# Optimization experiments

Hardware: AMD Instinct MI355X
Metric: run time of the kernel (lower is better)

Reference implementation:

```python
import jax, jax.numpy as jnp
import numpy as np

HIDDEN, INPUT_DIM, OUTPUT_DIM, SEQ_LEN, BATCH = 1024, 1, 10, 784, 512


def make_discrete_hippo(N, L):
    # HiPPO-LegS matrix: A[n,k] = -sqrt(2n+1)sqrt(2k+1) for n>k, -(n+1) on diag; B[n]=sqrt(2n+1)
    q = np.arange(N, dtype=np.float64)
    P = np.sqrt(1.0 + 2.0 * q)
    A = -(np.tril(np.outer(P, P)) - np.diag(q))
    B = P[:, None]  # (N, 1)
    # bilinear (Tustin) discretization with step = 1/L
    step = 1.0 / L
    I = np.eye(N)
    M = np.linalg.inv(I - (step / 2.0) * A)
    Ad = M @ (I + (step / 2.0) * A)
    Bd = step * (M @ B)
    return jnp.asarray(Ad, jnp.float32), jnp.asarray(Bd, jnp.float32)


def setup_inputs() -> dict:
    key = jax.random.key(0)
    k1, k2, k3 = jax.random.split(key, 3)
    x = jax.random.normal(k1, (BATCH, SEQ_LEN, 1), jnp.float32)
    # C: xavier_uniform-like scale, shape (input_dim, hidden_dim)
    C = jax.random.normal(k2, (INPUT_DIM, HIDDEN), jnp.float32) / np.sqrt(HIDDEN).astype(np.float32)
    # final Dense(output_dim): kernel (input_dim, output_dim), bias (output_dim,)
    W = jax.random.normal(k3, (INPUT_DIM, OUTPUT_DIM), jnp.float32)
    b = jnp.zeros((OUTPUT_DIM,), jnp.float32)
    return {"x": x, "C": C, "W": W, "b": b}


def reference(x, C, W, b):
    Ad, Bd = make_discrete_hippo(HIDDEN, SEQ_LEN)  # constants (not learned)
    AdT = Ad.T                       # (N, N)
    Bvec = Bd[:, 0]                  # (N,)
    us = jnp.moveaxis(x[..., 0], 1, 0)  # (seq, batch) -- scan over time axis
    h0 = jnp.zeros((x.shape[0], HIDDEN), x.dtype)

    def step(h, u):
        # h_next = tanh(A h^T + B u)^T  ==  tanh(h @ A^T + u[:,None]*B)
        h_next = jnp.tanh(h @ AdT + u[:, None] * Bvec[None, :])  # (batch, N)
        y = h_next @ C.T                                         # (batch, input_dim)
        return h_next, y

    _, ys = jax.lax.scan(step, h0, us)  # ys: (seq, batch, input_dim)
    # Dense applied to all timesteps then [:, -1, :] == Dense on last timestep
    return ys[-1] @ W + b  # (batch, output_dim)
```

## Files before the change

kernel.cpp:

```cpp
#include <hip/hip_runtime.h>
#include <math.h>


#define SEQ     784
#define OUT_DIM 10
#define NW      4
#define CH      16
#define NCH     (SEQ/CH)
#define EPL     4
#define NG      (EPL/2)

typedef float v2f __attribute__((ext_vector_type(2)));

#if __has_builtin(__builtin_elementwise_fma)
__device__ __forceinline__ v2f fma2(v2f a, v2f b, v2f c) {
    return __builtin_elementwise_fma(a, b, c);
}
#else
__device__ __forceinline__ v2f fma2(v2f a, v2f b, v2f c) {
    v2f r; r.x = fmaf(a.x, b.x, c.x); r.y = fmaf(a.y, b.y, c.y); return r;
}
#endif

#if __has_builtin(__builtin_amdgcn_exp2f)
#define EXP2F(x) __builtin_amdgcn_exp2f(x)
#else
#define EXP2F(x) __expf(0.69314718055994531f * (x))
#endif

template<int CTRL, int ROW_MASK>
__device__ __forceinline__ float dpp_mov(float src, float old) {
    return __int_as_float(__builtin_amdgcn_update_dpp(
        __float_as_int(old), __float_as_int(src), CTRL, ROW_MASK, 0xf, false));
}

__global__ __launch_bounds__(256, 2)
void ssm_hippo_scan(const float* __restrict__ x,
                    const float* __restrict__ C,
                    const float* __restrict__ W,
                    const float* __restrict__ bvec,
                    float* __restrict__ out)
{
    const int b    = blockIdx.x;
    const int tid  = threadIdx.x;
    const int wv   = tid >> 6;
    const int lane = tid & 63;

    __shared__ __align__(16) float u_s[SEQ];
    __shared__ __align__(16) float totB_s[NW-1][SEQ];
    __shared__ double part_s[NW];

    for (int t = tid; t < SEQ; t += 256) u_s[t] = x[b * SEQ + t];

    const double hdt  = 0.5 / (double)SEQ;
    const double L2E2 = 2.0 * 1.4426950408889634;

    v2f upc2[NG], nhdtP2[NG], pdin2[NG], invd2v[NG], aprod2[NG];
    v2f aprel2;
    float alphas[EPL], apH;
    float Alev0, Alev1, Alev2, Alev3, Alev4, Alev5, Aexcl;
    {
        double apd = 1.0;
#pragma unroll
        for (int i = 0; i < EPL; ++i) {
            const int    n = wv * 256 + lane * EPL + i;
            const double p = sqrt(1.0 + 2.0 * (double)n);
            const double d = 1.0 + hdt * (double)(n + 1);
            const double a = 1.0 - hdt * p * p / d;
            upc2[i>>1][i&1]   = (float)(L2E2 * hdt * p);
            nhdtP2[i>>1][i&1] = (float)(-hdt * p);
            pdin2[i>>1][i&1]  = (float)(p / d);
            invd2v[i>>1][i&1] = (float)(2.0 / d);
            alphas[i]         = (float)a;
            aprod2[i>>1][i&1] = (float)apd;
            apd *= a;
        }
        aprel2 = (v2f){1.0f, alphas[2]};
        apH    = alphas[2] * alphas[3];
        float A = (float)apd;
        Alev0 = A; A *= dpp_mov<0x111, 0xf>(A, 1.0f);
        Alev1 = A; A *= dpp_mov<0x112, 0xf>(A, 1.0f);
        Alev2 = A; A *= dpp_mov<0x114, 0xf>(A, 1.0f);
        Alev3 = A; A *= dpp_mov<0x118, 0xf>(A, 1.0f);
        Alev4 = A; A *= dpp_mov<0x142, 0xa>(A, 1.0f);
        Alev5 = A; A *= dpp_mov<0x143, 0xc>(A, 1.0f);
        Aexcl = dpp_mov<0x138, 0xf>(A, 1.0f);
    }

    float cF1 = 0.0f, cF2 = 0.0f, cF12 = 0.0f;
    {
        double n1 = 1.0, d1 = 1.0, n2 = 1.0, d2 = 1.0;
        for (int n = 256; n < 512; ++n) {
            n1 *= 1.0 - hdt * (double)n; d1 *= 1.0 + hdt * (double)(n + 1);
        }
        for (int n = 512; n < 768; ++n) {
            n2 *= 1.0 - hdt * (double)n; d2 *= 1.0 + hdt * (double)(n + 1);
        }
        const double Phi1 = n1 / d1, Phi2 = n2 / d2;
        cF1 = (float)Phi1; cF2 = (float)Phi2; cF12 = (float)(Phi1 * Phi2);
    }

    const float c2  = (float)L2E2;
    const float nc4 = (float)(-2.0 * L2E2);
    const float p4  = (float)(2.0 * L2E2);
    const v2f  c2v  = (v2f){c2, c2},  nc2v = (v2f){-c2, -c2};
    const v2f  nc4v = (v2f){nc4, nc4}, p4v = (v2f){p4, p4};

    __syncthreads();

    v2f r2[NG];
#pragma unroll
    for (int j = 0; j < NG; ++j) r2[j] = (v2f){0.5f, 0.5f};

#pragma unroll 1
    for (int tick = 0; tick < NCH + NW - 1; ++tick) {
        const int ch = tick - wv;
        if (0 <= ch && ch < NCH) {
            float4 u4[CH/4];
            float  Tin[CH];
            {
                const float4* up = (const float4*)&u_s[ch * CH];
#pragma unroll
                for (int q = 0; q < CH/4; ++q) u4[q] = up[q];
            }
            if (wv == 0) {
#pragma unroll
                for (int k = 0; k < CH; ++k) Tin[k] = 0.0f;
            } else if (wv == 1) {
                const float4* b0 = (const float4*)&totB_s[0][ch * CH];
#pragma unroll
                for (int q = 0; q < CH/4; ++q) {
                    const float4 v0 = b0[q];
                    Tin[4*q+0] = v0.x; Tin[4*q+1] = v0.y;
                    Tin[4*q+2] = v0.z; Tin[4*q+3] = v0.w;
                }
            } else if (wv == 2) {
                const float4* b0 = (const float4*)&totB_s[0][ch * CH];
                const float4* b1 = (const float4*)&totB_s[1][ch * CH];
#pragma unroll
                for (int q = 0; q < CH/4; ++q) {
                    const float4 v0 = b0[q], v1 = b1[q];
                    Tin[4*q+0] = fmaf(cF1, v0.x, v1.x);
                    Tin[4*q+1] = fmaf(cF1, v0.y, v1.y);
                    Tin[4*q+2] = fmaf(cF1, v0.z, v1.z);
                    Tin[4*q+3] = fmaf(cF1, v0.w, v1.w);
                }
            } else {
                const float4* b0 = (const float4*)&totB_s[0][ch * CH];
                const float4* b1 = (const float4*)&totB_s[1][ch * CH];
                const float4* b2 = (const float4*)&totB_s[2][ch * CH];
#pragma unroll
                for (int q = 0; q < CH/4; ++q) {
                    const float4 v0 = b0[q], v1 = b1[q], v2 = b2[q];
                    Tin[4*q+0] = fmaf(cF12, v0.x, fmaf(cF2, v1.x, v2.x));
                    Tin[4*q+1] = fmaf(cF12, v0.y, fmaf(cF2, v1.y, v2.y));
                    Tin[4*q+2] = fmaf(cF12, v0.z, fmaf(cF2, v1.z, v2.z));
                    Tin[4*q+3] = fmaf(cF12, v0.w, fmaf(cF2, v1.w, v2.w));
                }
            }
            float Bacc[CH];

#pragma unroll
            for (int k = 0; k < CH; ++k) {
                const float u  = ((const float*)&u4[k>>2])[k&3];
                const v2f  uu  = (v2f){u, u};

                v2f w2[NG], gam2[NG], negh[NG];
#pragma unroll
                for (int j = 0; j < NG; ++j) {
                    const v2f au = fma2(upc2[j], uu, c2v);
                    w2[j]   = fma2(nc4v, r2[j], au);
                    gam2[j] = pdin2[j] * w2[j];
                    negh[j] = fma2(p4v, r2[j], nc2v);
                }

                v2f Tb2[NG];
                Tb2[0] = (v2f){0.0f, gam2[0].x};
                const float Tl0 = fmaf(alphas[1], gam2[0].x, gam2[0].y);
                Tb2[1] = (v2f){0.0f, gam2[1].x};
                const float Tl1 = fmaf(alphas[3], gam2[1].x, gam2[1].y);
                Tb2[1] = fma2(aprel2, (v2f){Tl0, Tl0}, Tb2[1]);
                float B = fmaf(apH, Tl0, Tl1);

                float Bin;
                Bin = dpp_mov<0x111, 0xf>(B, 0.0f); B = fmaf(Alev0, Bin, B);
                Bin = dpp_mov<0x112, 0xf>(B, 0.0f); B = fmaf(Alev1, Bin, B);
                Bin = dpp_mov<0x114, 0xf>(B, 0.0f); B = fmaf(Alev2, Bin, B);
                Bin = dpp_mov<0x118, 0xf>(B, 0.0f); B = fmaf(Alev3, Bin, B);
                Bin = dpp_mov<0x142, 0xa>(B, 0.0f); B = fmaf(Alev4, Bin, B);
                Bin = dpp_mov<0x143, 0xc>(B, 0.0f); B = fmaf(Alev5, Bin, B);
                Bacc[k] = B;

                const float Tst  = dpp_mov<0x138, 0xf>(B, 0.0f);
                const float Tent = fmaf(Aexcl, Tin[k], Tst);
                const v2f  Tev   = (v2f){Tent, Tent};

                v2f Tn[NG], tmp[NG], g2l[NG], e[NG];
#pragma unroll
                for (int j = 0; j < NG; ++j) Tn[j]  = fma2(aprod2[j], Tev, Tb2[j]);
#pragma unroll
                for (int j = 0; j < NG; ++j) tmp[j] = fma2(nhdtP2[j], Tn[j], w2[j]);
#pragma unroll
                for (int j = 0; j < NG; ++j) g2l[j] = fma2(tmp[j], invd2v[j], negh[j]);
#pragma unroll
                for (int j = 0; j < NG; ++j) { e[j].x = EXP2F(g2l[j].x);
                                               e[j].y = EXP2F(g2l[j].y); }
#pragma unroll
                for (int j = 0; j < NG; ++j) e[j] = e[j] + (v2f){1.0f, 1.0f};
#pragma unroll
                for (int j = 0; j < NG; ++j) { r2[j].x = __builtin_amdgcn_rcpf(e[j].x);
                                               r2[j].y = __builtin_amdgcn_rcpf(e[j].y); }
            }

            if (wv < NW - 1 && lane == 63) {
                float4* tp = (float4*)&totB_s[wv][ch * CH];
#pragma unroll
                for (int q = 0; q < CH/4; ++q)
                    tp[q] = make_float4(Bacc[4*q], Bacc[4*q+1],
                                        Bacc[4*q+2], Bacc[4*q+3]);
            }
        }
        __syncthreads();
    }

    double acc = 0.0;
#pragma unroll
    for (int i = 0; i < EPL; ++i) {
        const float hi = fmaf(-2.0f, r2[i>>1][i&1], 1.0f);
        acc = fma((double)C[wv * 256 + lane * EPL + i], (double)hi, acc);
    }
#pragma unroll
    for (int off = 32; off > 0; off >>= 1)
        acc += __shfl_down(acc, off, 64);
    if (lane == 0) part_s[wv] = acc;
    __syncthreads();
    if (tid < OUT_DIM) {
        const double tot = part_s[0] + part_s[1] + part_s[2] + part_s[3];
        out[b * OUT_DIM + tid] =
            (float)fma(tot, (double)W[tid], (double)bvec[tid]);
    }
}

extern "C" void kernel_launch(void* const* d_in, const int* in_sizes, int n_in,
                              void* d_out, int out_size, void* d_ws, size_t ws_size,
                              hipStream_t stream) {
    const float* x  = (const float*)d_in[0];
    const float* C  = (const float*)d_in[1];
    const float* W  = (const float*)d_in[2];
    const float* bv = (const float*)d_in[3];
    float* out      = (float*)d_out;
    hipLaunchKernelGGL(ssm_hippo_scan, dim3(512), dim3(256), 0, stream,
                       x, C, W, bv, out);
}
```

Before: 265.8 us.

## Reformulate per-step recurrence with scaled state and shared reciprocal across four elements

Replaces the packed-float2 recurrence with a scalar reformulation: the state is kept as a scaled tanh value, and the intra-thread lower-triangular coupling is folded into precomputed coefficients. One reciprocal now serves four sigmoid denominators through product tricks, and most DPP moves switch to bound_ctrl broadcast. The aim is to cut transcendental and dependent-op count on the serial per-timestep critical path. In exchange it adds an fminf clamp before exp2 and gives up packed FMA. Combining four denominators into one product can also lose precision or overflow, which the clamp partly guards against.

```diff
diff --git a/kernel.cpp b/kernel.cpp
--- a/kernel.cpp
+++ b/kernel.cpp
@@ -8,19 +8,6 @@
 #define CH      16
 #define NCH     (SEQ/CH)
 #define EPL     4
-#define NG      (EPL/2)
-
-typedef float v2f __attribute__((ext_vector_type(2)));
-
-#if __has_builtin(__builtin_elementwise_fma)
-__device__ __forceinline__ v2f fma2(v2f a, v2f b, v2f c) {
-    return __builtin_elementwise_fma(a, b, c);
-}
-#else
-__device__ __forceinline__ v2f fma2(v2f a, v2f b, v2f c) {
-    v2f r; r.x = fmaf(a.x, b.x, c.x); r.y = fmaf(a.y, b.y, c.y); return r;
-}
-#endif
 
 #if __has_builtin(__builtin_amdgcn_exp2f)
 #define EXP2F(x) __builtin_amdgcn_exp2f(x)
@@ -32,6 +19,11 @@
 __device__ __forceinline__ float dpp_mov(float src, float old) {
     return __int_as_float(__builtin_amdgcn_update_dpp(
         __float_as_int(old), __float_as_int(src), CTRL, ROW_MASK, 0xf, false));
+}
+template<int CTRL>
+__device__ __forceinline__ float dpp_bc0(float src) {
+    return __int_as_float(__builtin_amdgcn_update_dpp(
+        0, __float_as_int(src), CTRL, 0xf, 0xf, true));
 }
 
 __global__ __launch_bounds__(256, 2)
@@ -55,29 +47,40 @@
     const double hdt  = 0.5 / (double)SEQ;
     const double L2E2 = 2.0 * 1.4426950408889634;
 
-    v2f upc2[NG], nhdtP2[NG], pdin2[NG], invd2v[NG], aprod2[NG];
-    v2f aprel2;
-    float alphas[EPL], apH;
+    float upc[EPL], ivd[EPL], ka[EPL], cB[EPL];
+    float t10, t20, t21, t30, t31, t32;
     float Alev0, Alev1, Alev2, Alev3, Alev4, Alev5, Aexcl;
+    float c2, n2c2;
     {
-        double apd = 1.0;
+        double p[EPL], d[EPL], a[EPL], pdin[EPL], hp[EPL];
 #pragma unroll
         for (int i = 0; i < EPL; ++i) {
-            const int    n = wv * 256 + lane * EPL + i;
-            const double p = sqrt(1.0 + 2.0 * (double)n);
-            const double d = 1.0 + hdt * (double)(n + 1);
-            const double a = 1.0 - hdt * p * p / d;
-            upc2[i>>1][i&1]   = (float)(L2E2 * hdt * p);
-            nhdtP2[i>>1][i&1] = (float)(-hdt * p);
-            pdin2[i>>1][i&1]  = (float)(p / d);
-            invd2v[i>>1][i&1] = (float)(2.0 / d);
-            alphas[i]         = (float)a;
-            aprod2[i>>1][i&1] = (float)apd;
-            apd *= a;
-        }
-        aprel2 = (v2f){1.0f, alphas[2]};
-        apH    = alphas[2] * alphas[3];
-        float A = (float)apd;
+            const int n = wv * 256 + lane * EPL + i;
+            p[i]    = sqrt(1.0 + 2.0 * (double)n);
+            d[i]    = 1.0 + hdt * (double)(n + 1);
+            a[i]    = 1.0 - hdt * p[i] * p[i] / d[i];
+            pdin[i] = p[i] / d[i];
+            hp[i]   = 2.0 * hdt * p[i] / d[i];
+            upc[i]  = (float)(L2E2 * hdt * p[i]);
+            ivd[i]  = (float)(2.0 / d[i]);
+        }
+        const double ap0 = 1.0, ap1 = a[0], ap2 = a[0]*a[1], ap3 = a[0]*a[1]*a[2];
+        ka[0] = (float)(-hp[0] * ap0);
+        ka[1] = (float)(-hp[1] * ap1);
+        ka[2] = (float)(-hp[2] * ap2);
+        ka[3] = (float)(-hp[3] * ap3);
+        cB[0] = (float)(a[1]*a[2]*a[3] * pdin[0]);
+        cB[1] = (float)(a[2]*a[3] * pdin[1]);
+        cB[2] = (float)(a[3] * pdin[2]);
+        cB[3] = (float)(pdin[3]);
+        t10 = (float)(-hp[1] * pdin[0]);
+        t20 = (float)(-hp[2] * a[1] * pdin[0]);
+        t21 = (float)(-hp[2] * pdin[1]);
+        t30 = (float)(-hp[3] * a[2] * a[1] * pdin[0]);
+        t31 = (float)(-hp[3] * a[2] * pdin[1]);
+        t32 = (float)(-hp[3] * pdin[2]);
+
+        float A = (float)(a[0]*a[1]*a[2]*a[3]);
         Alev0 = A; A *= dpp_mov<0x111, 0xf>(A, 1.0f);
         Alev1 = A; A *= dpp_mov<0x112, 0xf>(A, 1.0f);
         Alev2 = A; A *= dpp_mov<0x114, 0xf>(A, 1.0f);
@@ -85,6 +88,9 @@
         Alev4 = A; A *= dpp_mov<0x142, 0xa>(A, 1.0f);
         Alev5 = A; A *= dpp_mov<0x143, 0xc>(A, 1.0f);
         Aexcl = dpp_mov<0x138, 0xf>(A, 1.0f);
+
+        c2   = (float)L2E2;
+        n2c2 = (float)(-2.0 * L2E2);
     }
 
     float cF1 = 0.0f, cF2 = 0.0f, cF12 = 0.0f;
@@ -100,17 +106,9 @@
         cF1 = (float)Phi1; cF2 = (float)Phi2; cF12 = (float)(Phi1 * Phi2);
     }
 
-    const float c2  = (float)L2E2;
-    const float nc4 = (float)(-2.0 * L2E2);
-    const float p4  = (float)(2.0 * L2E2);
-    const v2f  c2v  = (v2f){c2, c2},  nc2v = (v2f){-c2, -c2};
-    const v2f  nc4v = (v2f){nc4, nc4}, p4v = (v2f){p4, p4};
-
     __syncthreads();
 
-    v2f r2[NG];
-#pragma unroll
-    for (int j = 0; j < NG; ++j) r2[j] = (v2f){0.5f, 0.5f};
+    float m0 = 0.0f, m1 = 0.0f, m2 = 0.0f, m3 = 0.0f;
 
 #pragma unroll 1
     for (int tick = 0; tick < NCH + NW - 1; ++tick) {
@@ -162,54 +160,55 @@
 
 #pragma unroll
             for (int k = 0; k < CH; ++k) {
-                const float u  = ((const float*)&u4[k>>2])[k&3];
-                const v2f  uu  = (v2f){u, u};
-
-                v2f w2[NG], gam2[NG], negh[NG];
-#pragma unroll
-                for (int j = 0; j < NG; ++j) {
-                    const v2f au = fma2(upc2[j], uu, c2v);
-                    w2[j]   = fma2(nc4v, r2[j], au);
-                    gam2[j] = pdin2[j] * w2[j];
-                    negh[j] = fma2(p4v, r2[j], nc2v);
-                }
-
-                v2f Tb2[NG];
-                Tb2[0] = (v2f){0.0f, gam2[0].x};
-                const float Tl0 = fmaf(alphas[1], gam2[0].x, gam2[0].y);
-                Tb2[1] = (v2f){0.0f, gam2[1].x};
-                const float Tl1 = fmaf(alphas[3], gam2[1].x, gam2[1].y);
-                Tb2[1] = fma2(aprel2, (v2f){Tl0, Tl0}, Tb2[1]);
-                float B = fmaf(apH, Tl0, Tl1);
+                const float u = ((const float*)&u4[k>>2])[k&3];
+
+                const float w0 = fmaf(upc[0], u, m0);
+                const float w1 = fmaf(upc[1], u, m1);
+                const float w2 = fmaf(upc[2], u, m2);
+                const float w3 = fmaf(upc[3], u, m3);
+
+                float B = fmaf(cB[0], w0,
+                          fmaf(cB[1], w1,
+                          fmaf(cB[2], w2, cB[3] * w3)));
 
                 float Bin;
-                Bin = dpp_mov<0x111, 0xf>(B, 0.0f); B = fmaf(Alev0, Bin, B);
-                Bin = dpp_mov<0x112, 0xf>(B, 0.0f); B = fmaf(Alev1, Bin, B);
-                Bin = dpp_mov<0x114, 0xf>(B, 0.0f); B = fmaf(Alev2, Bin, B);
-                Bin = dpp_mov<0x118, 0xf>(B, 0.0f); B = fmaf(Alev3, Bin, B);
+                Bin = dpp_bc0<0x111>(B);            B = fmaf(Alev0, Bin, B);
+                Bin = dpp_bc0<0x112>(B);            B = fmaf(Alev1, Bin, B);
+                Bin = dpp_bc0<0x114>(B);            B = fmaf(Alev2, Bin, B);
+                Bin = dpp_bc0<0x118>(B);            B = fmaf(Alev3, Bin, B);
                 Bin = dpp_mov<0x142, 0xa>(B, 0.0f); B = fmaf(Alev4, Bin, B);
                 Bin = dpp_mov<0x143, 0xc>(B, 0.0f); B = fmaf(Alev5, Bin, B);
                 Bacc[k] = B;
 
-                const float Tst  = dpp_mov<0x138, 0xf>(B, 0.0f);
+                const float Tst  = dpp_bc0<0x138>(B);
                 const float Tent = fmaf(Aexcl, Tin[k], Tst);
-                const v2f  Tev   = (v2f){Tent, Tent};
-
-                v2f Tn[NG], tmp[NG], g2l[NG], e[NG];
-#pragma unroll
-                for (int j = 0; j < NG; ++j) Tn[j]  = fma2(aprod2[j], Tev, Tb2[j]);
-#pragma unroll
-                for (int j = 0; j < NG; ++j) tmp[j] = fma2(nhdtP2[j], Tn[j], w2[j]);
-#pragma unroll
-                for (int j = 0; j < NG; ++j) g2l[j] = fma2(tmp[j], invd2v[j], negh[j]);
-#pragma unroll
-                for (int j = 0; j < NG; ++j) { e[j].x = EXP2F(g2l[j].x);
-                                               e[j].y = EXP2F(g2l[j].y); }
-#pragma unroll
-                for (int j = 0; j < NG; ++j) e[j] = e[j] + (v2f){1.0f, 1.0f};
-#pragma unroll
-                for (int j = 0; j < NG; ++j) { r2[j].x = __builtin_amdgcn_rcpf(e[j].x);
-                                               r2[j].y = __builtin_amdgcn_rcpf(e[j].y); }
+
+                const float b0g = fmaf(ivd[0], w0, -m0);
+                const float b1g = fmaf(ivd[1], w1, -m1);
+                const float b2g = fmaf(ivd[2], w2, -m2);
+                const float b3g = fmaf(ivd[3], w3, -m3);
+                const float g0 = fmaf(ka[0], Tent, b0g);
+                const float g1 = fmaf(ka[1], Tent, fmaf(t10, w0, b1g));
+                const float g2 = fmaf(ka[2], Tent,
+                                 fmaf(t20, w0, fmaf(t21, w1, b2g)));
+                const float g3 = fmaf(ka[3], Tent,
+                                 fmaf(t30, w0,
+                                 fmaf(t31, w1, fmaf(t32, w2, b3g))));
+
+                const float e0 = EXP2F(fminf(g0, 30.0f));
+                const float e1 = EXP2F(fminf(g1, 30.0f));
+                const float e2 = EXP2F(fminf(g2, 30.0f));
+                const float e3 = EXP2F(fminf(g3, 30.0f));
+                const float q0 = e0 + 1.0f, q1 = e1 + 1.0f;
+                const float q2 = e2 + 1.0f, q3 = e3 + 1.0f;
+                const float p01 = q0 * q1, p23 = q2 * q3;
+                const float ip  = __builtin_amdgcn_rcpf(p01 * p23);
+                const float i01 = p23 * ip;
+                const float i23 = p01 * ip;
+                m0 = fmaf(n2c2, q1 * i01, c2);
+                m1 = fmaf(n2c2, q0 * i01, c2);
+                m2 = fmaf(n2c2, q3 * i23, c2);
+                m3 = fmaf(n2c2, q2 * i23, c2);
             }
 
             if (wv < NW - 1 && lane == 63) {
@@ -224,10 +223,12 @@
     }
 
     double acc = 0.0;
-#pragma unroll
-    for (int i = 0; i < EPL; ++i) {
-        const float hi = fmaf(-2.0f, r2[i>>1][i&1], 1.0f);
-        acc = fma((double)C[wv * 256 + lane * EPL + i], (double)hi, acc);
+    {
+        const int base = wv * 256 + lane * EPL;
+        acc = fma((double)C[base + 0], (double)m0, acc);
+        acc = fma((double)C[base + 1], (double)m1, acc);
+        acc = fma((double)C[base + 2], (double)m2, acc);
+        acc = fma((double)C[base + 3], (double)m3, acc);
     }
 #pragma unroll
     for (int off = 32; off > 0; off >>= 1)
@@ -235,7 +236,8 @@
     if (lane == 0) part_s[wv] = acc;
     __syncthreads();
     if (tid < OUT_DIM) {
-        const double tot = part_s[0] + part_s[1] + part_s[2] + part_s[3];
+        const double tot = (part_s[0] + part_s[1] + part_s[2] + part_s[3])
+                         * 0.34657359027997264;
         out[b * OUT_DIM + tid] =
             (float)fma(tot, (double)W[tid], (double)bvec[tid]);
     }
```

Result: no change. 264.6 us (-0.5%).
